# Optimization experiments

Measured on AMD Instinct MI355X. Metric: run time of the kernel, lower is better.

The kernel has to match this reference:

```python
import jax, jax.numpy as jnp
import numpy as np

B, C, W, H = 16, 512, 32, 32


def spatial_shift1(y):
    # y: [B, W, H, C]; quartile-wise shifts with edge rows/cols left unchanged
    c = y.shape[-1]
    cq = c // 4
    p0 = jnp.concatenate([y[:, :1, :, 0*cq:1*cq], y[:, :-1, :, 0*cq:1*cq]], axis=1)  # w <- w-1
    p1 = jnp.concatenate([y[:, 1:, :, 1*cq:2*cq], y[:, -1:, :, 1*cq:2*cq]], axis=1)  # w <- w+1
    p2 = jnp.concatenate([y[:, :, :1, 2*cq:3*cq], y[:, :, :-1, 2*cq:3*cq]], axis=2)  # h <- h-1
    p3 = jnp.concatenate([y[:, :, 1:, 3*cq:], y[:, :, -1:, 3*cq:]], axis=2)          # h <- h+1
    return jnp.concatenate([p0, p1, p2, p3], axis=-1)


def spatial_shift2(y):
    # same as shift1 with w/h roles swapped
    c = y.shape[-1]
    cq = c // 4
    p0 = jnp.concatenate([y[:, :, :1, 0*cq:1*cq], y[:, :, :-1, 0*cq:1*cq]], axis=2)  # h <- h-1
    p1 = jnp.concatenate([y[:, :, 1:, 1*cq:2*cq], y[:, :, -1:, 1*cq:2*cq]], axis=2)  # h <- h+1
    p2 = jnp.concatenate([y[:, :1, :, 2*cq:3*cq], y[:, :-1, :, 2*cq:3*cq]], axis=1)  # w <- w-1
    p3 = jnp.concatenate([y[:, 1:, :, 3*cq:], y[:, -1:, :, 3*cq:]], axis=1)          # w <- w+1
    return jnp.concatenate([p0, p1, p2, p3], axis=-1)


def setup_inputs() -> dict:
    key = jax.random.key(0)
    ks = jax.random.split(key, 9)
    s = 0.02
    return {
        "x": jax.random.normal(ks[0], (B, C, W, H), dtype=jnp.float32),
        "w1": jax.random.normal(ks[1], (3 * C, C), dtype=jnp.float32) * s,
        "b1": jax.random.normal(ks[2], (3 * C,), dtype=jnp.float32) * s,
        "wa": jax.random.normal(ks[3], (C, C), dtype=jnp.float32) * s,
        "ba": jax.random.normal(ks[4], (C,), dtype=jnp.float32) * s,
        "wb": jax.random.normal(ks[5], (3 * C, C), dtype=jnp.float32) * s,
        "bb": jax.random.normal(ks[6], (3 * C,), dtype=jnp.float32) * s,
        "w2": jax.random.normal(ks[7], (C, C), dtype=jnp.float32) * s,
        "b2": jax.random.normal(ks[8], (C,), dtype=jnp.float32) * s,
    }


def reference(x, w1, b1, wa, ba, wb, bb, w2, b2):
    c = x.shape[1]
    xp = jnp.transpose(x, (0, 2, 3, 1))                     # [B, W, H, C]
    y = jnp.einsum("bwhc,oc->bwho", xp, w1) + b1            # [B, W, H, 3C]
    x1 = spatial_shift1(y[..., :c])
    x2 = spatial_shift2(y[..., c:2 * c])
    x3 = y[..., 2 * c:]
    # SplitAttention: descriptor a = sum over branches and spatial positions
    a = jnp.sum(x1 + x2 + x3, axis=(1, 2))                  # [B, C]
    hat = jax.nn.gelu(a @ wa.T + ba, approximate=False) @ wb.T + bb  # [B, 3C]
    bar = jax.nn.softmax(hat.reshape(-1, 3, c), axis=1)     # softmax over k=3
    g = bar[:, :, None, None, :]                            # [B, 3, 1, 1, C]
    out = g[:, 0] * x1 + g[:, 1] * x2 + g[:, 2] * x3        # [B, W, H, C]
    z = jnp.einsum("bwhc,oc->bwho", out, w2) + b2           # [B, W, H, C]
    return jnp.transpose(z, (0, 3, 1, 2))                   # [B, C, W, H]
```

## Files before the change

kernel.cpp:

```cpp
#include <hip/hip_runtime.h>
#include <stdint.h>

typedef __bf16 bf16x8 __attribute__((ext_vector_type(8)));
typedef float f32x4 __attribute__((ext_vector_type(4)));

#define B_ 16
#define C_ 512
#define S_ 1024
#define N1 1536

__device__ inline unsigned short f2b(float f) {
    unsigned int u = __builtin_bit_cast(unsigned int, f);
    unsigned int lsb = (u >> 16) & 1u;
    u += 0x7fffu + lsb;
    return (unsigned short)(u >> 16);
}
__device__ inline float b2f(unsigned int s) {
    unsigned int u = (s & 0xffffu) << 16;
    return __builtin_bit_cast(float, u);
}

__device__ inline void gl_lds16(const unsigned short* g, unsigned short* l) {
    __builtin_amdgcn_global_load_lds(
        (const __attribute__((address_space(1))) void*)(g),
        (__attribute__((address_space(3))) void*)(l),
        16, 0, 0);
}

__global__ void transpose_convert_x(const float* __restrict__ x, unsigned short* __restrict__ xT) {
    __shared__ float tile[32][33];
    int b = blockIdx.z;
    int c0 = blockIdx.y * 32;
    int s0 = blockIdx.x * 32;
    int tx = threadIdx.x, ty = threadIdx.y;
    const float* xp = x + ((size_t)b * C_ + c0) * S_ + s0;
#pragma unroll
    for (int i = 0; i < 4; i++)
        tile[ty + i * 8][tx] = xp[(size_t)(ty + i * 8) * S_ + tx];
    __syncthreads();
    unsigned short* op = xT + ((size_t)b * S_ + s0) * C_ + c0;
#pragma unroll
    for (int i = 0; i < 4; i++)
        op[(size_t)(ty + i * 8) * C_ + tx] = f2b(tile[tx][ty + i * 8]);
}

__global__ __launch_bounds__(256) void misc_prep(
    const float* __restrict__ w1, const float* __restrict__ w2,
    unsigned short* __restrict__ w1b, unsigned short* __restrict__ w2b,
    float* __restrict__ sums)
{
    int i = blockIdx.x * 256 + threadIdx.x;
    if (i < 196608) {
        float4 v = ((const float4*)w1)[i];
        ((ushort4*)w1b)[i] = make_ushort4(f2b(v.x), f2b(v.y), f2b(v.z), f2b(v.w));
    } else if (i < 262144) {
        int j = i - 196608;
        float4 v = ((const float4*)w2)[j];
        ((ushort4*)w2b)[j] = make_ushort4(f2b(v.x), f2b(v.y), f2b(v.z), f2b(v.w));
    } else if (i < 292864) {
        int j = i - 262144;
        ((float4*)sums)[j] = make_float4(0.f, 0.f, 0.f, 0.f);
    }
}

template <bool TRANS_OUT, bool DO_SUMS>
__global__ __launch_bounds__(256) void gemm_bf16(
    const unsigned short* __restrict__ A,
    const unsigned short* __restrict__ Wt,
    const float* __restrict__ bias,
    void* __restrict__ Cout, int N,
    float* __restrict__ Tsum, float* __restrict__ H0, float* __restrict__ H31,
    float* __restrict__ C0, float* __restrict__ C31)
{
    const int K = 512;
    __shared__ __align__(16) unsigned short As[128 * 32];
    __shared__ __align__(16) unsigned short Bs[128 * 32];
    int m0 = blockIdx.x * 128;
    int n0 = blockIdx.y * 128;
    int tid = threadIdx.x;
    int lane = tid & 63, wid = tid >> 6;
    int wm = (wid >> 1) * 64, wn = (wid & 1) * 64;
    int quad = lane >> 4, l16 = lane & 15;
    int ch0 = wid * 128 + lane;
    const unsigned short* Ab = A + (size_t)m0 * K;
    const unsigned short* Bb = Wt + (size_t)n0 * K;

    f32x4 acc[4][4] = {};

    for (int kt = 0; kt < K; kt += 32) {
        __syncthreads();
#pragma unroll
        for (int i = 0; i < 2; i++) {
            int ch = ch0 + i * 64;
            int m = ch >> 2, kc = ch & 3;
            size_t go = (size_t)m * K + kt + kc * 8;
            gl_lds16(Ab + go, &As[ch * 8]);
            gl_lds16(Bb + go, &Bs[ch * 8]);
        }
        __syncthreads();
        bf16x8 af[4], bfr[4];
#pragma unroll
        for (int t = 0; t < 4; t++) {
            af[t]  = *(const bf16x8*)&As[(wm + t * 16 + l16) * 32 + quad * 8];
            bfr[t] = *(const bf16x8*)&Bs[(wn + t * 16 + l16) * 32 + quad * 8];
        }
#pragma unroll
        for (int mt = 0; mt < 4; mt++)
#pragma unroll
            for (int nt = 0; nt < 4; nt++)
                acc[mt][nt] = __builtin_amdgcn_mfma_f32_16x16x32_bf16(af[mt], bfr[nt], acc[mt][nt], 0, 0, 0);
    }

#pragma unroll
    for (int mt = 0; mt < 4; mt++) {
#pragma unroll
        for (int nt = 0; nt < 4; nt++) {
            int n = n0 + wn + nt * 16 + l16;
            float bv = bias[n];
            int mbase = m0 + wm + mt * 16 + quad * 4;
            if (!TRANS_OUT) {
                unsigned short* Y = (unsigned short*)Cout;
#pragma unroll
                for (int r = 0; r < 4; r++)
                    Y[(size_t)(mbase + r) * N + n] = f2b(acc[mt][nt][r] + bv);
            } else {
                float* Z = (float*)Cout;
                int b = mbase >> 10;
                int s = mbase & 1023;
                float4 v = make_float4(acc[mt][nt][0] + bv, acc[mt][nt][1] + bv,
                                       acc[mt][nt][2] + bv, acc[mt][nt][3] + bv);
                *(float4*)(&Z[((size_t)(b * 512 + n)) * 1024 + s]) = v;
            }
        }
    }

    if (DO_SUMS) {
        int b = m0 >> 10;
        int wlo = (m0 & 1023) >> 5;
#pragma unroll
        for (int nt = 0; nt < 4; nt++) {
            int n = n0 + wn + nt * 16 + l16;
            float bv = bias[n];
            float tT = 0.f;
#pragma unroll
            for (int mt = 0; mt < 4; mt++)
#pragma unroll
                for (int r = 0; r < 4; r++) tT += acc[mt][nt][r] + bv;
            tT += __shfl_xor(tT, 16);
            tT += __shfl_xor(tT, 32);
            if (quad == 0) {
                atomicAdd(&Tsum[b * 1536 + n], tT);
                float th0 = acc[0][nt][0] + acc[2][nt][0] + 2.f * bv;
                atomicAdd(&H0[b * 1536 + n], th0);
            }
            if (quad == 3) {
                float th31 = acc[1][nt][3] + acc[3][nt][3] + 2.f * bv;
                atomicAdd(&H31[b * 1536 + n], th31);
            }
            if (wlo == 0 && wm == 0) {
                float tc = 0.f;
#pragma unroll
                for (int mt = 0; mt < 2; mt++)
#pragma unroll
                    for (int r = 0; r < 4; r++) tc += acc[mt][nt][r] + bv;
                tc += __shfl_xor(tc, 16);
                tc += __shfl_xor(tc, 32);
                if (quad == 0) atomicAdd(&C0[b * 1536 + n], tc);
            }
            if (wlo == 28 && wm == 64) {
                float tc = 0.f;
#pragma unroll
                for (int mt = 2; mt < 4; mt++)
#pragma unroll
                    for (int r = 0; r < 4; r++) tc += acc[mt][nt][r] + bv;
                tc += __shfl_xor(tc, 16);
                tc += __shfl_xor(tc, 32);
                if (quad == 0) atomicAdd(&C31[b * 1536 + n], tc);
            }
        }
    }
}

__global__ __launch_bounds__(256) void mlp_layer1(
    const float* __restrict__ sums, const float* __restrict__ wa,
    const float* __restrict__ ba, float* __restrict__ h)
{
    __shared__ float sa[512];
    int b = blockIdx.x >> 7;
    int t = threadIdx.x;
    const float* Tp   = sums;
    const float* H0p  = sums + 24576;
    const float* H31p = sums + 49152;
    const float* C0p  = sums + 73728;
    const float* C31p = sums + 98304;
#pragma unroll
    for (int j = 0; j < 2; j++) {
        int c = t + j * 256;
        int q = c >> 7;
        int n1 = b * 1536 + c;
        float t123 = Tp[n1] + Tp[n1 + 512] + Tp[n1 + 1024];
        float sC1 = C0p[n1] - C31p[n1];
        float sH1 = H0p[n1] - H31p[n1];
        float sC2 = C0p[n1 + 512] - C31p[n1 + 512];
        float sH2 = H0p[n1 + 512] - H31p[n1 + 512];
        float e = (q < 2) ? (sC1 + sH2) : (sH1 + sC2);
        sa[c] = t123 + ((q & 1) ? -e : e);
    }
    __syncthreads();
    int lane = t & 63, wid = t >> 6;
    int o = (blockIdx.x & 127) * 4 + wid;
    const float4* wr = (const float4*)(wa + (size_t)o * 512);
    float4 w0 = wr[lane * 2], w1v = wr[lane * 2 + 1];
    float4 a0 = ((const float4*)sa)[lane * 2], a1 = ((const float4*)sa)[lane * 2 + 1];
    float dot = w0.x * a0.x + w0.y * a0.y + w0.z * a0.z + w0.w * a0.w
              + w1v.x * a1.x + w1v.y * a1.y + w1v.z * a1.z + w1v.w * a1.w;
#pragma unroll
    for (int off = 32; off; off >>= 1) dot += __shfl_down(dot, off);
    if (lane == 0) {
        float v = dot + ba[o];
        h[b * 512 + o] = 0.5f * v * (1.0f + erff(v * 0.7071067811865475f));
    }
}

__global__ __launch_bounds__(256) void mlp_layer2(
    const float* __restrict__ h, const float* __restrict__ wb,
    const float* __restrict__ bb, float* __restrict__ hat)
{
    int gw = (blockIdx.x * 256 + threadIdx.x) >> 6;
    int lane = threadIdx.x & 63;
    int b = gw / 1536;
    int o = gw - b * 1536;
    const float4* wr = (const float4*)(wb + (size_t)o * 512);
    const float4* hr = (const float4*)(h + (size_t)b * 512);
    float4 w0 = wr[lane * 2], w1 = wr[lane * 2 + 1];
    float4 h0 = hr[lane * 2], h1 = hr[lane * 2 + 1];
    float dot = w0.x * h0.x + w0.y * h0.y + w0.z * h0.z + w0.w * h0.w
              + w1.x * h1.x + w1.y * h1.y + w1.z * h1.z + w1.w * h1.w;
#pragma unroll
    for (int off = 32; off; off >>= 1) dot += __shfl_down(dot, off);
    if (lane == 0)
        hat[(size_t)b * 1536 + o] = dot + bb[o];
}

__global__ __launch_bounds__(256) void combine_softmax(
    const unsigned short* __restrict__ y, const float* __restrict__ hat,
    unsigned short* __restrict__ outT)
{
    int b = blockIdx.y;
    int t = threadIdx.x;
    int w = blockIdx.x * 4 + (t >> 6);
    int c8 = (t & 63) * 8;
    int q = c8 >> 7;
    int dw1 = (q == 0) ? -1 : (q == 1) ? 1 : 0;
    int dh1 = (q == 2) ? -1 : (q == 3) ? 1 : 0;
    int dh2 = (q == 0) ? -1 : (q == 1) ? 1 : 0;
    int dw2 = (q == 2) ? -1 : (q == 3) ? 1 : 0;
    float g0[8], g1[8], g2[8];
#pragma unroll
    for (int j = 0; j < 8; j++) {
        int c = c8 + j;
        float h0 = hat[b * 1536 + c];
        float h1 = hat[b * 1536 + 512 + c];
        float h2 = hat[b * 1536 + 1024 + c];
        float mx = fmaxf(h0, fmaxf(h1, h2));
        float e0 = __expf(h0 - mx), e1 = __expf(h1 - mx), e2 = __expf(h2 - mx);
        float inv = 1.0f / (e0 + e1 + e2);
        g0[j] = e0 * inv; g1[j] = e1 * inv; g2[j] = e2 * inv;
    }
    int w1i = min(max(w + dw1, 0), 31);
    int w2i = min(max(w + dw2, 0), 31);
    size_t base = (size_t)b * S_;
    for (int h = 0; h < 32; h++) {
        int h1i = min(max(h + dh1, 0), 31);
        int h2i = min(max(h + dh2, 0), 31);
        uint4 u1 = *(const uint4*)&y[(base + w1i * 32 + h1i) * N1 + c8];
        uint4 u2 = *(const uint4*)&y[(base + w2i * 32 + h2i) * N1 + 512 + c8];
        uint4 u3 = *(const uint4*)&y[(base + w * 32 + h) * N1 + 1024 + c8];
        unsigned int p[4];
        const unsigned int* a1 = &u1.x;
        const unsigned int* a2 = &u2.x;
        const unsigned int* a3 = &u3.x;
#pragma unroll
        for (int k = 0; k < 4; k++) {
            int j = k * 2;
            float lo = g0[j] * b2f(a1[k]) + g1[j] * b2f(a2[k]) + g2[j] * b2f(a3[k]);
            float hi = g0[j + 1] * b2f(a1[k] >> 16) + g1[j + 1] * b2f(a2[k] >> 16) + g2[j + 1] * b2f(a3[k] >> 16);
            p[k] = (unsigned int)f2b(lo) | ((unsigned int)f2b(hi) << 16);
        }
        *(uint4*)&outT[(base + w * 32 + h) * 512 + c8] = make_uint4(p[0], p[1], p[2], p[3]);
    }
}

extern "C" void kernel_launch(void* const* d_in, const int* in_sizes, int n_in,
                              void* d_out, int out_size, void* d_ws, size_t ws_size,
                              hipStream_t stream) {
    const float* x  = (const float*)d_in[0];
    const float* w1 = (const float*)d_in[1];
    const float* b1 = (const float*)d_in[2];
    const float* wa = (const float*)d_in[3];
    const float* ba = (const float*)d_in[4];
    const float* wb = (const float*)d_in[5];
    const float* bb = (const float*)d_in[6];
    const float* w2 = (const float*)d_in[7];
    const float* b2 = (const float*)d_in[8];
    float* out = (float*)d_out;

    char* ws = (char*)d_ws;
    unsigned short* xT   = (unsigned short*)(ws);
    unsigned short* outT = (unsigned short*)(ws);
    unsigned short* w1b  = (unsigned short*)(ws + 16777216);
    unsigned short* w2b  = (unsigned short*)(ws + 18350080);
    unsigned short* y    = (unsigned short*)(ws + 18874368);
    float* sums          = (float*)(ws + 69206016);
    float* h_buf         = (float*)(ws + 69697536);
    float* hat_buf       = (float*)(ws + 69730304);

    float* Tsum = sums;
    float* H0   = sums + 24576;
    float* H31  = sums + 49152;
    float* C0   = sums + 73728;
    float* C31  = sums + 98304;

    transpose_convert_x<<<dim3(32, 16, 16), dim3(32, 8), 0, stream>>>(x, xT);
    misc_prep<<<dim3(1144), dim3(256), 0, stream>>>(w1, w2, w1b, w2b, sums);
    gemm_bf16<false, true><<<dim3(128, 12), dim3(256), 0, stream>>>(
        xT, w1b, b1, (void*)y, 1536, Tsum, H0, H31, C0, C31);
    mlp_layer1<<<dim3(2048), dim3(256), 0, stream>>>(sums, wa, ba, h_buf);
    mlp_layer2<<<dim3(6144), dim3(256), 0, stream>>>(h_buf, wb, bb, hat_buf);
    combine_softmax<<<dim3(8, 16), dim3(256), 0, stream>>>(y, hat_buf, outT);
    gemm_bf16<true, false><<<dim3(128, 4), dim3(256), 0, stream>>>(
        outT, w2b, b2, (void*)out, 512, nullptr, nullptr, nullptr, nullptr, nullptr);
}
```

Before: 193.4 us.

## Fuse shift-combine into second GEMM A-load and merge prep and softmax kernels

Builds the gated, shifted combination of the three branches directly in the second GEMM's shared-memory A tile, so the bf16 outT intermediate is never written to or read back from global memory. The layer-2 MLP and the 3-way softmax become one kernel that keeps wb rows in registers across batches and writes gates. The transpose and weight-conversion prep kernels are merged into one launch. In exchange, each of the four N-tile blocks recomputes the combine and issues three scattered y loads per row through regular loads rather than async LDS loads, and mlp2 runs on only 128 blocks.

```diff
diff --git a/kernel.cpp b/kernel.cpp
--- a/kernel.cpp
+++ b/kernel.cpp
@@ -27,52 +27,58 @@
         16, 0, 0);
 }
 
-__global__ void transpose_convert_x(const float* __restrict__ x, unsigned short* __restrict__ xT) {
-    __shared__ float tile[32][33];
-    int b = blockIdx.z;
-    int c0 = blockIdx.y * 32;
-    int s0 = blockIdx.x * 32;
-    int tx = threadIdx.x, ty = threadIdx.y;
-    const float* xp = x + ((size_t)b * C_ + c0) * S_ + s0;
-#pragma unroll
-    for (int i = 0; i < 4; i++)
-        tile[ty + i * 8][tx] = xp[(size_t)(ty + i * 8) * S_ + tx];
-    __syncthreads();
-    unsigned short* op = xT + ((size_t)b * S_ + s0) * C_ + c0;
-#pragma unroll
-    for (int i = 0; i < 4; i++)
-        op[(size_t)(ty + i * 8) * C_ + tx] = f2b(tile[tx][ty + i * 8]);
-}
-
-__global__ __launch_bounds__(256) void misc_prep(
+__global__ __launch_bounds__(256) void prep_all(
+    const float* __restrict__ x, unsigned short* __restrict__ xT,
     const float* __restrict__ w1, const float* __restrict__ w2,
     unsigned short* __restrict__ w1b, unsigned short* __restrict__ w2b,
     float* __restrict__ sums)
 {
-    int i = blockIdx.x * 256 + threadIdx.x;
-    if (i < 196608) {
-        float4 v = ((const float4*)w1)[i];
-        ((ushort4*)w1b)[i] = make_ushort4(f2b(v.x), f2b(v.y), f2b(v.z), f2b(v.w));
-    } else if (i < 262144) {
-        int j = i - 196608;
-        float4 v = ((const float4*)w2)[j];
-        ((ushort4*)w2b)[j] = make_ushort4(f2b(v.x), f2b(v.y), f2b(v.z), f2b(v.w));
-    } else if (i < 292864) {
-        int j = i - 262144;
-        ((float4*)sums)[j] = make_float4(0.f, 0.f, 0.f, 0.f);
-    }
-}
-
-template <bool TRANS_OUT, bool DO_SUMS>
-__global__ __launch_bounds__(256) void gemm_bf16(
+    int bid = blockIdx.x;
+    int t = threadIdx.x;
+    if (bid < 8192) {
+        __shared__ float tile[32][33];
+        int bx = bid & 31;
+        int by = (bid >> 5) & 15;
+        int bz = bid >> 9;
+        int c0 = by * 32;
+        int s0 = bx * 32;
+        int tx = t & 31, ty = t >> 5;
+        const float* xp = x + ((size_t)bz * C_ + c0) * S_ + s0;
+#pragma unroll
+        for (int i = 0; i < 4; i++)
+            tile[ty + i * 8][tx] = xp[(size_t)(ty + i * 8) * S_ + tx];
+        __syncthreads();
+        unsigned short* op = xT + ((size_t)bz * S_ + s0) * C_ + c0;
+#pragma unroll
+        for (int i = 0; i < 4; i++)
+            op[(size_t)(ty + i * 8) * C_ + tx] = f2b(tile[tx][ty + i * 8]);
+    } else {
+        int i = (bid - 8192) * 256 + t;
+        if (i < 196608) {
+            float4 v = ((const float4*)w1)[i];
+            ((ushort4*)w1b)[i] = make_ushort4(f2b(v.x), f2b(v.y), f2b(v.z), f2b(v.w));
+        } else if (i < 262144) {
+            int j = i - 196608;
+            float4 v = ((const float4*)w2)[j];
+            ((ushort4*)w2b)[j] = make_ushort4(f2b(v.x), f2b(v.y), f2b(v.z), f2b(v.w));
+        } else if (i < 292864) {
+            int j = i - 262144;
+            ((float4*)sums)[j] = make_float4(0.f, 0.f, 0.f, 0.f);
+        }
+    }
+}
+
+
+__global__ __launch_bounds__(256) void gemm1(
     const unsigned short* __restrict__ A,
     const unsigned short* __restrict__ Wt,
     const float* __restrict__ bias,
-    void* __restrict__ Cout, int N,
+    unsigned short* __restrict__ Y,
     float* __restrict__ Tsum, float* __restrict__ H0, float* __restrict__ H31,
     float* __restrict__ C0, float* __restrict__ C31)
 {
     const int K = 512;
+    const int N = 1536;
     __shared__ __align__(16) unsigned short As[128 * 32];
     __shared__ __align__(16) unsigned short Bs[128 * 32];
     int m0 = blockIdx.x * 128;
@@ -118,23 +124,13 @@
             int n = n0 + wn + nt * 16 + l16;
             float bv = bias[n];
             int mbase = m0 + wm + mt * 16 + quad * 4;
-            if (!TRANS_OUT) {
-                unsigned short* Y = (unsigned short*)Cout;
-#pragma unroll
-                for (int r = 0; r < 4; r++)
-                    Y[(size_t)(mbase + r) * N + n] = f2b(acc[mt][nt][r] + bv);
-            } else {
-                float* Z = (float*)Cout;
-                int b = mbase >> 10;
-                int s = mbase & 1023;
-                float4 v = make_float4(acc[mt][nt][0] + bv, acc[mt][nt][1] + bv,
-                                       acc[mt][nt][2] + bv, acc[mt][nt][3] + bv);
-                *(float4*)(&Z[((size_t)(b * 512 + n)) * 1024 + s]) = v;
-            }
-        }
-    }
-
-    if (DO_SUMS) {
+#pragma unroll
+            for (int r = 0; r < 4; r++)
+                Y[(size_t)(mbase + r) * N + n] = f2b(acc[mt][nt][r] + bv);
+        }
+    }
+
+    {
         int b = m0 >> 10;
         int wlo = (m0 & 1023) >> 5;
 #pragma unroll
@@ -222,72 +218,154 @@
     }
 }
 
-__global__ __launch_bounds__(256) void mlp_layer2(
+__global__ __launch_bounds__(256) void mlp2_gate(
     const float* __restrict__ h, const float* __restrict__ wb,
-    const float* __restrict__ bb, float* __restrict__ hat)
+    const float* __restrict__ bb, float* __restrict__ g)
 {
-    int gw = (blockIdx.x * 256 + threadIdx.x) >> 6;
-    int lane = threadIdx.x & 63;
-    int b = gw / 1536;
-    int o = gw - b * 1536;
-    const float4* wr = (const float4*)(wb + (size_t)o * 512);
-    const float4* hr = (const float4*)(h + (size_t)b * 512);
-    float4 w0 = wr[lane * 2], w1 = wr[lane * 2 + 1];
-    float4 h0 = hr[lane * 2], h1 = hr[lane * 2 + 1];
-    float dot = w0.x * h0.x + w0.y * h0.y + w0.z * h0.z + w0.w * h0.w
-              + w1.x * h1.x + w1.y * h1.y + w1.z * h1.z + w1.w * h1.w;
-#pragma unroll
-    for (int off = 32; off; off >>= 1) dot += __shfl_down(dot, off);
-    if (lane == 0)
-        hat[(size_t)b * 1536 + o] = dot + bb[o];
-}
-
-__global__ __launch_bounds__(256) void combine_softmax(
-    const unsigned short* __restrict__ y, const float* __restrict__ hat,
-    unsigned short* __restrict__ outT)
-{
-    int b = blockIdx.y;
-    int t = threadIdx.x;
-    int w = blockIdx.x * 4 + (t >> 6);
-    int c8 = (t & 63) * 8;
-    int q = c8 >> 7;
-    int dw1 = (q == 0) ? -1 : (q == 1) ? 1 : 0;
-    int dh1 = (q == 2) ? -1 : (q == 3) ? 1 : 0;
-    int dh2 = (q == 0) ? -1 : (q == 1) ? 1 : 0;
-    int dw2 = (q == 2) ? -1 : (q == 3) ? 1 : 0;
-    float g0[8], g1[8], g2[8];
-#pragma unroll
-    for (int j = 0; j < 8; j++) {
-        int c = c8 + j;
-        float h0 = hat[b * 1536 + c];
-        float h1 = hat[b * 1536 + 512 + c];
-        float h2 = hat[b * 1536 + 1024 + c];
+    __shared__ float hat_s[4][3][16];
+    int wv = threadIdx.x >> 6, lane = threadIdx.x & 63;
+    int c = blockIdx.x * 4 + wv;
+    float4 wr[3][2];
+    float bbv[3];
+#pragma unroll
+    for (int j = 0; j < 3; j++) {
+        const float4* p = (const float4*)(wb + (size_t)(j * 512 + c) * 512 + lane * 8);
+        wr[j][0] = p[0]; wr[j][1] = p[1];
+        bbv[j] = bb[j * 512 + c];
+    }
+    for (int b = 0; b < 16; b++) {
+        const float4* hp = (const float4*)(h + b * 512 + lane * 8);
+        float4 h0 = hp[0], h1 = hp[1];
+        float d[3];
+#pragma unroll
+        for (int j = 0; j < 3; j++) {
+            d[j] = wr[j][0].x * h0.x + wr[j][0].y * h0.y + wr[j][0].z * h0.z + wr[j][0].w * h0.w
+                 + wr[j][1].x * h1.x + wr[j][1].y * h1.y + wr[j][1].z * h1.z + wr[j][1].w * h1.w;
+#pragma unroll
+            for (int off = 32; off; off >>= 1) d[j] += __shfl_down(d[j], off);
+        }
+        if (lane == 0) {
+#pragma unroll
+            for (int j = 0; j < 3; j++) hat_s[wv][j][b] = d[j] + bbv[j];
+        }
+    }
+    __syncthreads();
+    if (lane < 16) {
+        int b = lane;
+        float h0 = hat_s[wv][0][b], h1 = hat_s[wv][1][b], h2 = hat_s[wv][2][b];
         float mx = fmaxf(h0, fmaxf(h1, h2));
         float e0 = __expf(h0 - mx), e1 = __expf(h1 - mx), e2 = __expf(h2 - mx);
         float inv = 1.0f / (e0 + e1 + e2);
-        g0[j] = e0 * inv; g1[j] = e1 * inv; g2[j] = e2 * inv;
-    }
-    int w1i = min(max(w + dw1, 0), 31);
-    int w2i = min(max(w + dw2, 0), 31);
-    size_t base = (size_t)b * S_;
-    for (int h = 0; h < 32; h++) {
-        int h1i = min(max(h + dh1, 0), 31);
-        int h2i = min(max(h + dh2, 0), 31);
-        uint4 u1 = *(const uint4*)&y[(base + w1i * 32 + h1i) * N1 + c8];
-        uint4 u2 = *(const uint4*)&y[(base + w2i * 32 + h2i) * N1 + 512 + c8];
-        uint4 u3 = *(const uint4*)&y[(base + w * 32 + h) * N1 + 1024 + c8];
-        unsigned int p[4];
-        const unsigned int* a1 = &u1.x;
-        const unsigned int* a2 = &u2.x;
-        const unsigned int* a3 = &u3.x;
-#pragma unroll
-        for (int k = 0; k < 4; k++) {
-            int j = k * 2;
-            float lo = g0[j] * b2f(a1[k]) + g1[j] * b2f(a2[k]) + g2[j] * b2f(a3[k]);
-            float hi = g0[j + 1] * b2f(a1[k] >> 16) + g1[j + 1] * b2f(a2[k] >> 16) + g2[j + 1] * b2f(a3[k] >> 16);
-            p[k] = (unsigned int)f2b(lo) | ((unsigned int)f2b(hi) << 16);
-        }
-        *(uint4*)&outT[(base + w * 32 + h) * 512 + c8] = make_uint4(p[0], p[1], p[2], p[3]);
+        g[(b * 3 + 0) * 512 + c] = e0 * inv;
+        g[(b * 3 + 1) * 512 + c] = e1 * inv;
+        g[(b * 3 + 2) * 512 + c] = e2 * inv;
+    }
+}
+
+__global__ __launch_bounds__(256) void gemm2_fused(
+    const unsigned short* __restrict__ y,
+    const float* __restrict__ g,
+    const unsigned short* __restrict__ Wt,
+    const float* __restrict__ bias,
+    float* __restrict__ Z)
+{
+    const int K = 512;
+    __shared__ __align__(16) unsigned short As[128 * 32];
+    __shared__ __align__(16) unsigned short Bs[128 * 32];
+    int m0 = blockIdx.x * 128;
+    int n0 = blockIdx.y * 128;
+    int tid = threadIdx.x;
+    int lane = tid & 63, wid = tid >> 6;
+    int wm = (wid >> 1) * 64, wn = (wid & 1) * 64;
+    int quad = lane >> 4, l16 = lane & 15;
+    int ch0 = wid * 128 + lane;
+    const unsigned short* Bb = Wt + (size_t)n0 * K;
+
+    int b = m0 >> 10;
+    int m_l = tid >> 1;
+    int half = tid & 1;
+    int s = (m0 & 1023) + m_l;
+    int w = s >> 5, hh = s & 31;
+    size_t ybase = (size_t)b * 1024;
+    const float* gA = g + (b * 3 + 0) * 512;
+    const float* gB = g + (b * 3 + 1) * 512;
+    const float* gC = g + (b * 3 + 2) * 512;
+
+    f32x4 acc[4][4] = {};
+
+    for (int kt = 0; kt < K; kt += 32) {
+        __syncthreads();
+#pragma unroll
+        for (int i = 0; i < 2; i++) {
+            int ch = ch0 + i * 64;
+            int m = ch >> 2, kc = ch & 3;
+            gl_lds16(Bb + (size_t)m * K + kt + kc * 8, &Bs[ch * 8]);
+        }
+        {
+            int q = kt >> 7;
+            int dw1 = (q == 0) ? -1 : (q == 1) ? 1 : 0;
+            int dh1 = (q == 2) ? -1 : (q == 3) ? 1 : 0;
+            int dh2 = (q == 0) ? -1 : (q == 1) ? 1 : 0;
+            int dw2 = (q == 2) ? -1 : (q == 3) ? 1 : 0;
+            int w1i = min(max(w + dw1, 0), 31), h1i = min(max(hh + dh1, 0), 31);
+            int w2i = min(max(w + dw2, 0), 31), h2i = min(max(hh + dh2, 0), 31);
+            const unsigned short* y1p = y + (ybase + w1i * 32 + h1i) * N1 + kt;
+            const unsigned short* y2p = y + (ybase + w2i * 32 + h2i) * N1 + 512 + kt;
+            const unsigned short* y3p = y + (ybase + w * 32 + hh) * N1 + 1024 + kt;
+            int c0 = half * 16;
+#pragma unroll
+            for (int cc = 0; cc < 2; cc++) {
+                int cb = c0 + cc * 8;
+                uint4 u1 = *(const uint4*)(y1p + cb);
+                uint4 u2 = *(const uint4*)(y2p + cb);
+                uint4 u3 = *(const uint4*)(y3p + cb);
+                float4 ga0 = *(const float4*)(gA + kt + cb), ga1 = *(const float4*)(gA + kt + cb + 4);
+                float4 gb0 = *(const float4*)(gB + kt + cb), gb1 = *(const float4*)(gB + kt + cb + 4);
+                float4 gc0 = *(const float4*)(gC + kt + cb), gc1 = *(const float4*)(gC + kt + cb + 4);
+                const unsigned int* a1 = &u1.x;
+                const unsigned int* a2 = &u2.x;
+                const unsigned int* a3 = &u3.x;
+                const float* pga[2] = { &ga0.x, &ga1.x };
+                const float* pgb[2] = { &gb0.x, &gb1.x };
+                const float* pgc[2] = { &gc0.x, &gc1.x };
+                unsigned int pk[4];
+#pragma unroll
+                for (int k4 = 0; k4 < 4; k4++) {
+                    int gi = k4 >> 1, go_ = (k4 & 1) * 2;
+                    float lo = pga[gi][go_]     * b2f(a1[k4])       + pgb[gi][go_]     * b2f(a2[k4])       + pgc[gi][go_]     * b2f(a3[k4]);
+                    float hi = pga[gi][go_ + 1] * b2f(a1[k4] >> 16) + pgb[gi][go_ + 1] * b2f(a2[k4] >> 16) + pgc[gi][go_ + 1] * b2f(a3[k4] >> 16);
+                    pk[k4] = (unsigned int)f2b(lo) | ((unsigned int)f2b(hi) << 16);
+                }
+                *(uint4*)&As[m_l * 32 + cb] = make_uint4(pk[0], pk[1], pk[2], pk[3]);
+            }
+        }
+        __syncthreads();
+        bf16x8 af[4], bfr[4];
+#pragma unroll
+        for (int t = 0; t < 4; t++) {
+            af[t]  = *(const bf16x8*)&As[(wm + t * 16 + l16) * 32 + quad * 8];
+            bfr[t] = *(const bf16x8*)&Bs[(wn + t * 16 + l16) * 32 + quad * 8];
+        }
+#pragma unroll
+        for (int mt = 0; mt < 4; mt++)
+#pragma unroll
+            for (int nt = 0; nt < 4; nt++)
+                acc[mt][nt] = __builtin_amdgcn_mfma_f32_16x16x32_bf16(af[mt], bfr[nt], acc[mt][nt], 0, 0, 0);
+    }
+
+#pragma unroll
+    for (int mt = 0; mt < 4; mt++) {
+#pragma unroll
+        for (int nt = 0; nt < 4; nt++) {
+            int n = n0 + wn + nt * 16 + l16;
+            float bv = bias[n];
+            int mbase = m0 + wm + mt * 16 + quad * 4;
+            int bb_ = mbase >> 10;
+            int ss = mbase & 1023;
+            float4 v = make_float4(acc[mt][nt][0] + bv, acc[mt][nt][1] + bv,
+                                   acc[mt][nt][2] + bv, acc[mt][nt][3] + bv);
+            *(float4*)(&Z[((size_t)(bb_ * 512 + n)) * 1024 + ss]) = v;
+        }
     }
 }
 
@@ -307,13 +385,12 @@
 
     char* ws = (char*)d_ws;
     unsigned short* xT   = (unsigned short*)(ws);
-    unsigned short* outT = (unsigned short*)(ws);
     unsigned short* w1b  = (unsigned short*)(ws + 16777216);
     unsigned short* w2b  = (unsigned short*)(ws + 18350080);
     unsigned short* y    = (unsigned short*)(ws + 18874368);
     float* sums          = (float*)(ws + 69206016);
     float* h_buf         = (float*)(ws + 69697536);
-    float* hat_buf       = (float*)(ws + 69730304);
+    float* g_buf         = (float*)(ws + 69730304);
 
     float* Tsum = sums;
     float* H0   = sums + 24576;
@@ -321,13 +398,10 @@
     float* C0   = sums + 73728;
     float* C31  = sums + 98304;
 
-    transpose_convert_x<<<dim3(32, 16, 16), dim3(32, 8), 0, stream>>>(x, xT);
-    misc_prep<<<dim3(1144), dim3(256), 0, stream>>>(w1, w2, w1b, w2b, sums);
-    gemm_bf16<false, true><<<dim3(128, 12), dim3(256), 0, stream>>>(
-        xT, w1b, b1, (void*)y, 1536, Tsum, H0, H31, C0, C31);
+    prep_all<<<dim3(9336), dim3(256), 0, stream>>>(x, xT, w1, w2, w1b, w2b, sums);
+    gemm1<<<dim3(128, 12), dim3(256), 0, stream>>>(
+        xT, w1b, b1, y, Tsum, H0, H31, C0, C31);
     mlp_layer1<<<dim3(2048), dim3(256), 0, stream>>>(sums, wa, ba, h_buf);
-    mlp_layer2<<<dim3(6144), dim3(256), 0, stream>>>(h_buf, wb, bb, hat_buf);
-    combine_softmax<<<dim3(8, 16), dim3(256), 0, stream>>>(y, hat_buf, outT);
-    gemm_bf16<true, false><<<dim3(128, 4), dim3(256), 0, stream>>>(
-        outT, w2b, b2, (void*)out, 512, nullptr, nullptr, nullptr, nullptr, nullptr);
-}
+    mlp2_gate<<<dim3(128), dim3(256), 0, stream>>>(h_buf, wb, bb, g_buf);
+    gemm2_fused<<<dim3(128, 4), dim3(256), 0, stream>>>(y, g_buf, w2b, b2, out);
+}
```

New measurement: 200.7 us. +3.8%, slower.
